# Kernel optimization log

Measured on AMD Instinct MI355X. Metric: run time of the kernel, lower is better.

## Reference

```python
import jax, jax.numpy as jnp
import numpy as np

SIGMA_DATA = 16.0
ALPHA_BOND = 1.0


def safe_norm(x, axis=-1):
    # L2 norm with zero (sub)gradient at 0, matching torch.norm's behavior
    sq = jnp.sum(x * x, axis=axis)
    n = jnp.sqrt(jnp.where(sq > 0, sq, 1.0))
    return jnp.where(sq > 0, n, 0.0)


def weighted_rigid_align(x_l, xGT_l, w_l):
    # Aligns x_l onto xGT_l's frame (Kabsch with weights); output is detached.
    wm = w_l[..., None]                                   # [B,N,1]
    denom = jnp.sum(wm, axis=1, keepdims=True)
    mu = jnp.sum(wm * x_l, axis=1, keepdims=True) / denom
    muGT = jnp.sum(wm * xGT_l, axis=1, keepdims=True) / denom
    xc = x_l - mu
    xGTc = xGT_l - muGT
    # M = (w * xGT_c)^T @ x_c  -> [B,3,3]
    M = jnp.einsum('bni,bnj->bij', wm * xGTc, xc)
    U, S, Vh = jnp.linalg.svd(M)
    R = U @ Vh
    det = jnp.linalg.det(R)
    Fm = jnp.array([[1.0, 0.0, 0.0], [0.0, 1.0, 0.0], [0.0, 0.0, -1.0]], dtype=R.dtype)
    Rfix = jnp.einsum('bij,jk,bkl->bil', U, Fm, Vh)
    R = jnp.where(det[:, None, None] < 0, Rfix, R)
    xalign = xc @ jnp.swapaxes(R, -1, -2) + muGT
    return jax.lax.stop_gradient(xalign)


def diffusion_loss(xpred_l, xGT_l, ht, w_l):
    # Align ground truth onto prediction (note arg order in original forward)
    xGT_aligned = weighted_rigid_align(xGT_l, xpred_l, w_l)
    loss = jnp.sum(safe_norm(xpred_l - xGT_aligned) * w_l) / jnp.sum(w_l)
    if ALPHA_BOND > 0:
        w_pair = w_l[:, :, None] * w_l[:, None, :]                 # [B,N,N]
        d_pred = safe_norm(xpred_l[:, :, None] - xpred_l[:, None]) # [B,N,N]
        d_gt = safe_norm(xGT_l[:, :, None] - xGT_l[:, None])       # [B,N,N]
        L_bond = w_pair * (d_pred - d_gt) ** 2
        loss = loss + ALPHA_BOND * jnp.sum(L_bond) / jnp.sum(w_pair)
    return (ht ** 2 + SIGMA_DATA ** 2) / (ht + SIGMA_DATA) ** 2 * loss


def setup_inputs() -> dict:
    key = jax.random.key(0)
    k1, k2, k3, k4 = jax.random.split(key, 4)
    B, N = 4, 2048
    xpred_l = jax.random.normal(k1, (B, N, 3), dtype=jnp.float32) * 10.0
    xGT_l = jax.random.normal(k2, (B, N, 3), dtype=jnp.float32) * 10.0
    ht = jax.random.uniform(k3, (B,), dtype=jnp.float32, minval=0.1, maxval=4.0)
    w_l = jax.random.uniform(k4, (B, N), dtype=jnp.float32, minval=0.1, maxval=1.0)
    return {"xpred_l": xpred_l, "xGT_l": xGT_l, "ht": ht, "w_l": w_l}


def reference(xpred_l, xGT_l, ht, w_l):
    return diffusion_loss(xpred_l, xGT_l, ht, w_l)
```

## Files before the change

kernel.cpp:

```cpp
#include <hip/hip_runtime.h>
#include <math.h>


#define RT 256
#define CT 64
#define MAXB 8

__global__ __launch_bounds__(RT, 4)
void k_main(const float* __restrict__ pred, const float* __restrict__ gt,
            const float* __restrict__ ht, const float* __restrict__ w,
            float* __restrict__ out, double* __restrict__ ws,
            int N, int B, unsigned total) {
    const int b   = blockIdx.z;
    const int r0  = blockIdx.x * RT;
    const int c0  = blockIdx.y * CT;
    const int tid = threadIdx.x;
    const int lane = tid & 63, wave = tid >> 6;
    const float* p  = pred + (size_t)b * N * 3;
    const float* g  = gt   + (size_t)b * N * 3;
    const float* wb = w    + (size_t)b * N;
    double* stats = ws + (size_t)b * 16;
    double* bondp = ws + 16 * B;
    unsigned* cnt = (unsigned*)(ws + 16 * B + 1);

    __shared__ float4 sp4[CT], sg4[CT];
    __shared__ double shred[4][16];

    const bool bond_active = (c0 + CT > r0 + 1);

    const int n = r0 + tid;
    const bool row_ok = (n < N);
    float px=0.f,py=0.f,pz=0.f,gx=0.f,gy=0.f,gz=0.f,wn=0.f;
    if (row_ok) {
        px = p[3*n]; py = p[3*n+1]; pz = p[3*n+2];
        gx = g[3*n]; gy = g[3*n+1]; gz = g[3*n+2];
        wn = wb[n];
    }

    if (bond_active) {
        for (int i = tid; i < CT; i += RT) {
            int m = c0 + i;
            if (m < N) {
                sp4[i] = make_float4(p[3*m], p[3*m+1], p[3*m+2], wb[m]);
                sg4[i] = make_float4(g[3*m], g[3*m+1], g[3*m+2], 0.0f);
            } else {
                sp4[i] = make_float4(0.f,0.f,0.f,0.f);
                sg4[i] = make_float4(0.f,0.f,0.f,0.f);
            }
        }
        __syncthreads();
    }

    float bond_f = 0.0f;
    if (bond_active && row_ok && (c0 + CT - 1 > n)) {
        int cc = min(CT, N - c0);
        for (int i = 0; i < cc; i++) {
            float4 cp = sp4[i];
            float4 cg = sg4[i];
            float dxp = px-cp.x, dyp = py-cp.y, dzp = pz-cp.z;
            float dp  = sqrtf(dxp*dxp + dyp*dyp + dzp*dzp);
            float dxg = gx-cg.x, dyg = gy-cg.y, dzg = gz-cg.z;
            float dg  = sqrtf(dxg*dxg + dyg*dyg + dzg*dzg);
            float dd  = dp - dg;
            float t   = wn * cp.w * dd * dd;
            bond_f += (c0 + i > n) ? t : 0.0f;
        }
    }
    bond_f *= 2.0f;

    if (blockIdx.y == 0) {
        double wd = (double)wn;
        double pxd=px, pyd=py, pzd=pz, gxd=gx, gyd=gy, gzd=gz;
        double st[16];
        st[0]=wd;
        st[1]=wd*pxd;  st[2]=wd*pyd;  st[3]=wd*pzd;
        st[4]=wd*gxd;  st[5]=wd*gyd;  st[6]=wd*gzd;
        st[7]=wd*pxd*gxd;  st[8]=wd*pxd*gyd;  st[9]=wd*pxd*gzd;
        st[10]=wd*pyd*gxd; st[11]=wd*pyd*gyd; st[12]=wd*pyd*gzd;
        st[13]=wd*pzd*gxd; st[14]=wd*pzd*gyd; st[15]=wd*pzd*gzd;
        #pragma unroll
        for (int off = 32; off > 0; off >>= 1) {
            #pragma unroll
            for (int k = 0; k < 16; k++) st[k] += __shfl_down(st[k], off, 64);
        }
        if (lane == 0) {
            #pragma unroll
            for (int k = 0; k < 16; k++) shred[wave][k] = st[k];
        }
        __syncthreads();
        if (tid < 16) {
            double s = shred[0][tid]+shred[1][tid]+shred[2][tid]+shred[3][tid];
            unsafeAtomicAdd(&stats[tid], s);
        }
    }

    double bd = (double)bond_f;
    #pragma unroll
    for (int off = 32; off > 0; off >>= 1) bd += __shfl_down(bd, off, 64);
    __syncthreads();
    if (lane == 0) shred[wave][0] = bd;
    __syncthreads();
    if (tid == 0) {
        double bt = shred[0][0]+shred[1][0]+shred[2][0]+shred[3][0];
        unsafeAtomicAdd(bondp, bt);
    }

    __shared__ int s_last;
    __syncthreads();
    if (tid == 0) {
        __threadfence();
        unsigned old = atomicAdd(cnt, 1u);
        s_last = (old == total - 1u) ? 1 : 0;
    }
    __syncthreads();
    if (!s_last) return;

    __shared__ double Rm[MAXB][16];
    if (tid < B) {
        double s[16];
        double* sb = ws + (size_t)tid * 16;
        for (int k = 0; k < 16; k++) s[k] = unsafeAtomicAdd(&sb[k], 0.0);
        double W = s[0];
        double mup[3] = { s[1]/W, s[2]/W, s[3]/W };
        double mug[3] = { s[4]/W, s[5]/W, s[6]/W };
        double M[3][3];
        for (int i = 0; i < 3; i++)
            for (int j = 0; j < 3; j++)
                M[i][j] = s[7 + i*3 + j] - W * mup[i] * mug[j];

        double A[3][3];
        for (int i = 0; i < 3; i++)
            for (int j = 0; j < 3; j++) {
                double t = 0.0;
                for (int k = 0; k < 3; k++) t += M[k][i] * M[k][j];
                A[i][j] = t;
            }
        double V[3][3] = {{1,0,0},{0,1,0},{0,0,1}};
        for (int sweep = 0; sweep < 8; sweep++) {
            for (int pq = 0; pq < 3; pq++) {
                int pp_ = (pq == 2) ? 1 : 0;
                int qq_ = (pq == 0) ? 1 : 2;
                double apq = A[pp_][qq_];
                if (fabs(apq) < 1e-300) continue;
                double app = A[pp_][pp_], aqq = A[qq_][qq_];
                double theta = (aqq - app) / (2.0 * apq);
                double t = copysign(1.0, theta) / (fabs(theta) + sqrt(theta*theta + 1.0));
                double c = 1.0 / sqrt(t*t + 1.0), sn = t * c;
                A[pp_][pp_] = app - t * apq;
                A[qq_][qq_] = aqq + t * apq;
                A[pp_][qq_] = A[qq_][pp_] = 0.0;
                int r = 3 - pp_ - qq_;
                double arp = A[r][pp_], arq = A[r][qq_];
                A[r][pp_] = A[pp_][r] = c*arp - sn*arq;
                A[r][qq_] = A[qq_][r] = sn*arp + c*arq;
                for (int rr = 0; rr < 3; rr++) {
                    double vp = V[rr][pp_], vq = V[rr][qq_];
                    V[rr][pp_] = c*vp - sn*vq;
                    V[rr][qq_] = sn*vp + c*vq;
                }
            }
        }
        double d[3] = { A[0][0], A[1][1], A[2][2] };
        int idx[3] = {0, 1, 2};
        for (int i = 0; i < 2; i++)
            for (int j = i + 1; j < 3; j++)
                if (d[idx[j]] > d[idx[i]]) { int tt = idx[i]; idx[i] = idx[j]; idx[j] = tt; }
        double u[3][3], v[3][3];
        for (int i = 0; i < 3; i++) {
            int c_ = idx[i];
            double sv = sqrt(fmax(d[c_], 0.0));
            double inv = (sv > 1e-12) ? 1.0 / sv : 0.0;
            for (int r = 0; r < 3; r++) v[i][r] = V[r][c_];
            for (int r = 0; r < 3; r++) {
                double t = 0.0;
                for (int k = 0; k < 3; k++) t += M[r][k] * v[i][k];
                u[i][r] = t * inv;
            }
        }
        double detM = M[0][0]*(M[1][1]*M[2][2] - M[1][2]*M[2][1])
                    - M[0][1]*(M[1][0]*M[2][2] - M[1][2]*M[2][0])
                    + M[0][2]*(M[1][0]*M[2][1] - M[1][1]*M[2][0]);
        double sg2 = (detM < 0.0) ? -1.0 : 1.0;
        double* o = Rm[tid];
        for (int r = 0; r < 3; r++)
            for (int cc2 = 0; cc2 < 3; cc2++)
                o[r*3 + cc2] = u[0][r]*v[0][cc2] + u[1][r]*v[1][cc2] + sg2 * u[2][r]*v[2][cc2];
        for (int i = 0; i < 3; i++) o[9 + i]  = mup[i];
        for (int i = 0; i < 3; i++) o[12 + i] = mug[i];
        o[15] = W;
    }
    __syncthreads();

    double al = 0.0;
    for (int idx2 = tid; idx2 < B * N; idx2 += RT) {
        int bb = idx2 / N, nn = idx2 - bb * N;
        const float* pp = pred + ((size_t)bb * N + nn) * 3;
        const float* gg = gt   + ((size_t)bb * N + nn) * 3;
        double wv = w[(size_t)bb * N + nn];
        const double* o = Rm[bb];
        double xc0 = (double)gg[0]-o[12], xc1 = (double)gg[1]-o[13], xc2 = (double)gg[2]-o[14];
        double ax = o[0]*xc0 + o[1]*xc1 + o[2]*xc2 + o[9];
        double ay = o[3]*xc0 + o[4]*xc1 + o[5]*xc2 + o[10];
        double az = o[6]*xc0 + o[7]*xc1 + o[8]*xc2 + o[11];
        double ex = (double)pp[0]-ax, ey = (double)pp[1]-ay, ez = (double)pp[2]-az;
        double sq = ex*ex + ey*ey + ez*ez;
        al += (sq > 0.0) ? wv * sqrt(sq) : 0.0;
    }
    #pragma unroll
    for (int off = 32; off > 0; off >>= 1) al += __shfl_down(al, off, 64);
    __syncthreads();
    if (lane == 0) shred[wave][1] = al;
    __syncthreads();
    __shared__ double s_loss;
    if (tid == 0) {
        double at = shred[0][1]+shred[1][1]+shred[2][1]+shred[3][1];
        double tw = 0.0, twp = 0.0;
        for (int i = 0; i < B; i++) { double W = Rm[i][15]; tw += W; twp += W*W; }
        double bond = unsafeAtomicAdd(bondp, 0.0);
        s_loss = at / tw + bond / twp;
    }
    __syncthreads();
    if (tid < B) {
        double h = (double)ht[tid];
        out[tid] = (float)(((h*h + 256.0) / ((h + 16.0)*(h + 16.0))) * s_loss);
    }
}

extern "C" void kernel_launch(void* const* d_in, const int* in_sizes, int n_in,
                              void* d_out, int out_size, void* d_ws, size_t ws_size,
                              hipStream_t stream) {
    const float* pred = (const float*)d_in[0];
    const float* gt   = (const float*)d_in[1];
    const float* ht   = (const float*)d_in[2];
    const float* w    = (const float*)d_in[3];
    int B = in_sizes[2];
    int N = in_sizes[3] / B;
    double* ws = (double*)d_ws;
    float* out = (float*)d_out;

    hipMemsetAsync(d_ws, 0, (size_t)(16 * B + 2) * sizeof(double), stream);

    dim3 grid((N + RT - 1) / RT, (N + CT - 1) / CT, B);
    unsigned total = grid.x * grid.y * grid.z;
    k_main<<<grid, dim3(RT), 0, stream>>>(pred, gt, ht, w, out, ws, N, B, total);
}
```

Measured before the change: 107.7 us.

## Widen column tiles, split bond loop by diagonal, use per-block partial slots

Doubles the column tile width to halve the block count, and splits the bond loop into an unmasked path for tiles fully above the diagonal and a masked path for diagonal tiles. Replaces same-address atomics with per-block partial slots that the last block reduces, drops the threadfence, and computes the final alignment term in float with per-batch rotation hoisted out of the loop. It aims to cut contended atomics, block launch overhead and the serialized double-precision tail. In exchange it zeroes a larger workspace, needs shared staging that limits B*GX, and loses some precision in the float alignment sum.

```diff
diff --git a/kernel.cpp b/kernel.cpp
--- a/kernel.cpp
+++ b/kernel.cpp
@@ -3,32 +3,36 @@
 
 
 #define RT 256
-#define CT 64
+#define CT 128
 #define MAXB 8
+#define MAXSTAT 1024
 
 __global__ __launch_bounds__(RT, 4)
 void k_main(const float* __restrict__ pred, const float* __restrict__ gt,
             const float* __restrict__ ht, const float* __restrict__ w,
             float* __restrict__ out, double* __restrict__ ws,
             int N, int B, unsigned total) {
-    const int b   = blockIdx.z;
-    const int r0  = blockIdx.x * RT;
-    const int c0  = blockIdx.y * CT;
-    const int tid = threadIdx.x;
+    const int b    = blockIdx.z;
+    const int bx   = blockIdx.x;
+    const int r0   = bx * RT;
+    const int c0   = blockIdx.y * CT;
+    const int tid  = threadIdx.x;
     const int lane = tid & 63, wave = tid >> 6;
+    const int GX   = gridDim.x;
+    const unsigned linear = (blockIdx.z * gridDim.y + blockIdx.y) * GX + blockIdx.x;
+
+    double* statsSlot = ws;
+    double* bondSlot  = ws + (size_t)B * GX * 16;
+    unsigned* cnt     = (unsigned*)(bondSlot + total);
+
     const float* p  = pred + (size_t)b * N * 3;
     const float* g  = gt   + (size_t)b * N * 3;
     const float* wb = w    + (size_t)b * N;
-    double* stats = ws + (size_t)b * 16;
-    double* bondp = ws + 16 * B;
-    unsigned* cnt = (unsigned*)(ws + 16 * B + 1);
 
     __shared__ float4 sp4[CT], sg4[CT];
     __shared__ double shred[4][16];
 
-    const bool bond_active = (c0 + CT > r0 + 1);
-
-    const int n = r0 + tid;
+    const int  n      = r0 + tid;
     const bool row_ok = (n < N);
     float px=0.f,py=0.f,pz=0.f,gx=0.f,gy=0.f,gz=0.f,wn=0.f;
     if (row_ok) {
@@ -37,47 +41,53 @@
         wn = wb[n];
     }
 
+    const bool bond_active = (c0 + CT > r0 + 1) && (c0 < N);
+    float bond_f = 0.0f;
     if (bond_active) {
         for (int i = tid; i < CT; i += RT) {
             int m = c0 + i;
+            float4 a = make_float4(0.f,0.f,0.f,0.f), c = a;
             if (m < N) {
-                sp4[i] = make_float4(p[3*m], p[3*m+1], p[3*m+2], wb[m]);
-                sg4[i] = make_float4(g[3*m], g[3*m+1], g[3*m+2], 0.0f);
-            } else {
-                sp4[i] = make_float4(0.f,0.f,0.f,0.f);
-                sg4[i] = make_float4(0.f,0.f,0.f,0.f);
-            }
+                a = make_float4(p[3*m], p[3*m+1], p[3*m+2], wb[m]);
+                c = make_float4(g[3*m], g[3*m+1], g[3*m+2], 0.f);
+            }
+            sp4[i] = a; sg4[i] = c;
         }
         __syncthreads();
-    }
-
-    float bond_f = 0.0f;
-    if (bond_active && row_ok && (c0 + CT - 1 > n)) {
-        int cc = min(CT, N - c0);
-        for (int i = 0; i < cc; i++) {
-            float4 cp = sp4[i];
-            float4 cg = sg4[i];
-            float dxp = px-cp.x, dyp = py-cp.y, dzp = pz-cp.z;
-            float dp  = sqrtf(dxp*dxp + dyp*dyp + dzp*dzp);
-            float dxg = gx-cg.x, dyg = gy-cg.y, dzg = gz-cg.z;
-            float dg  = sqrtf(dxg*dxg + dyg*dyg + dzg*dzg);
-            float dd  = dp - dg;
-            float t   = wn * cp.w * dd * dd;
-            bond_f += (c0 + i > n) ? t : 0.0f;
+        if (row_ok) {
+            const int cc = min(CT, N - c0);
+            if (c0 >= r0 + RT) {
+                for (int i = 0; i < cc; i++) {
+                    float4 cp = sp4[i], cg = sg4[i];
+                    float dxp=px-cp.x, dyp=py-cp.y, dzp=pz-cp.z;
+                    float dxg=gx-cg.x, dyg=gy-cg.y, dzg=gz-cg.z;
+                    float dp = sqrtf(dxp*dxp+dyp*dyp+dzp*dzp);
+                    float dg = sqrtf(dxg*dxg+dyg*dyg+dzg*dzg);
+                    float dd = dp - dg;
+                    bond_f += (wn*cp.w)*(dd*dd);
+                }
+            } else if (n < c0 + cc - 1) {
+                for (int i = 0; i < cc; i++) {
+                    float4 cp = sp4[i], cg = sg4[i];
+                    float dxp=px-cp.x, dyp=py-cp.y, dzp=pz-cp.z;
+                    float dxg=gx-cg.x, dyg=gy-cg.y, dzg=gz-cg.z;
+                    float dp = sqrtf(dxp*dxp+dyp*dyp+dzp*dzp);
+                    float dg = sqrtf(dxg*dxg+dyg*dyg+dzg*dzg);
+                    float dd = dp - dg;
+                    float t  = (wn*cp.w)*(dd*dd);
+                    bond_f += (c0 + i > n) ? t : 0.0f;
+                }
+            }
         }
     }
     bond_f *= 2.0f;
 
     if (blockIdx.y == 0) {
-        double wd = (double)wn;
-        double pxd=px, pyd=py, pzd=pz, gxd=gx, gyd=gy, gzd=gz;
-        double st[16];
-        st[0]=wd;
-        st[1]=wd*pxd;  st[2]=wd*pyd;  st[3]=wd*pzd;
-        st[4]=wd*gxd;  st[5]=wd*gyd;  st[6]=wd*gzd;
-        st[7]=wd*pxd*gxd;  st[8]=wd*pxd*gyd;  st[9]=wd*pxd*gzd;
-        st[10]=wd*pyd*gxd; st[11]=wd*pyd*gyd; st[12]=wd*pyd*gzd;
-        st[13]=wd*pzd*gxd; st[14]=wd*pzd*gyd; st[15]=wd*pzd*gzd;
+        double wd=wn, pxd=px,pyd=py,pzd=pz, gxd=gx,gyd=gy,gzd=gz;
+        double st[16] = {wd, wd*pxd, wd*pyd, wd*pzd, wd*gxd, wd*gyd, wd*gzd,
+                         wd*pxd*gxd, wd*pxd*gyd, wd*pxd*gzd,
+                         wd*pyd*gxd, wd*pyd*gyd, wd*pyd*gzd,
+                         wd*pzd*gxd, wd*pzd*gyd, wd*pzd*gzd};
         #pragma unroll
         for (int off = 32; off > 0; off >>= 1) {
             #pragma unroll
@@ -90,36 +100,52 @@
         __syncthreads();
         if (tid < 16) {
             double s = shred[0][tid]+shred[1][tid]+shred[2][tid]+shred[3][tid];
-            unsafeAtomicAdd(&stats[tid], s);
-        }
+            unsafeAtomicAdd(&statsSlot[((size_t)b*GX + bx)*16 + tid], s);
+        }
+        __syncthreads();
     }
 
     double bd = (double)bond_f;
     #pragma unroll
     for (int off = 32; off > 0; off >>= 1) bd += __shfl_down(bd, off, 64);
-    __syncthreads();
     if (lane == 0) shred[wave][0] = bd;
     __syncthreads();
-    if (tid == 0) {
+    if (tid == 0 && bond_active) {
         double bt = shred[0][0]+shred[1][0]+shred[2][0]+shred[3][0];
-        unsafeAtomicAdd(bondp, bt);
-    }
-
-    __shared__ int s_last;
-    __syncthreads();
-    if (tid == 0) {
-        __threadfence();
-        unsigned old = atomicAdd(cnt, 1u);
-        s_last = (old == total - 1u) ? 1 : 0;
-    }
-    __syncthreads();
-    if (!s_last) return;
-
-    __shared__ double Rm[MAXB][16];
+        unsafeAtomicAdd(&bondSlot[linear], bt);
+    }
+
+    __shared__ unsigned s_old;
+    __syncthreads();
+    if (tid == 0) s_old = atomicAdd(cnt, 1u);
+    __syncthreads();
+    if (s_old != total - 1u) return;
+
+    const int nstat = B * GX * 16;
+    __shared__ double sstat[MAXSTAT];
+    for (int i = tid; i < nstat; i += RT)
+        sstat[i] = unsafeAtomicAdd(&statsSlot[i], 0.0);
+
+    double bsum = 0.0;
+    for (unsigned i = tid; i < total; i += RT)
+        bsum += unsafeAtomicAdd(&bondSlot[i], 0.0);
+    #pragma unroll
+    for (int off = 32; off > 0; off >>= 1) bsum += __shfl_down(bsum, off, 64);
+    if (lane == 0) shred[wave][1] = bsum;
+    __syncthreads();
+
+    __shared__ double s_bond;
+    __shared__ float  Rf[MAXB][15];
+    __shared__ double Wd[MAXB];
+    if (tid == 0) s_bond = shred[0][1]+shred[1][1]+shred[2][1]+shred[3][1];
+
     if (tid < B) {
         double s[16];
-        double* sb = ws + (size_t)tid * 16;
-        for (int k = 0; k < 16; k++) s[k] = unsafeAtomicAdd(&sb[k], 0.0);
+        for (int k = 0; k < 16; k++) {
+            double acc = 0.0;
+            for (int j = 0; j < GX; j++) acc += sstat[((size_t)tid*GX + j)*16 + k];
+            s[k] = acc;
+        }
         double W = s[0];
         double mup[3] = { s[1]/W, s[2]/W, s[3]/W };
         double mug[3] = { s[4]/W, s[5]/W, s[6]/W };
@@ -145,18 +171,18 @@
                 double app = A[pp_][pp_], aqq = A[qq_][qq_];
                 double theta = (aqq - app) / (2.0 * apq);
                 double t = copysign(1.0, theta) / (fabs(theta) + sqrt(theta*theta + 1.0));
-                double c = 1.0 / sqrt(t*t + 1.0), sn = t * c;
+                double cj = 1.0 / sqrt(t*t + 1.0), sn = t * cj;
                 A[pp_][pp_] = app - t * apq;
                 A[qq_][qq_] = aqq + t * apq;
                 A[pp_][qq_] = A[qq_][pp_] = 0.0;
                 int r = 3 - pp_ - qq_;
                 double arp = A[r][pp_], arq = A[r][qq_];
-                A[r][pp_] = A[pp_][r] = c*arp - sn*arq;
-                A[r][qq_] = A[qq_][r] = sn*arp + c*arq;
+                A[r][pp_] = A[pp_][r] = cj*arp - sn*arq;
+                A[r][qq_] = A[qq_][r] = sn*arp + cj*arq;
                 for (int rr = 0; rr < 3; rr++) {
                     double vp = V[rr][pp_], vq = V[rr][qq_];
-                    V[rr][pp_] = c*vp - sn*vq;
-                    V[rr][qq_] = sn*vp + c*vq;
+                    V[rr][pp_] = cj*vp - sn*vq;
+                    V[rr][qq_] = sn*vp + cj*vq;
                 }
             }
         }
@@ -181,43 +207,47 @@
                     - M[0][1]*(M[1][0]*M[2][2] - M[1][2]*M[2][0])
                     + M[0][2]*(M[1][0]*M[2][1] - M[1][1]*M[2][0]);
         double sg2 = (detM < 0.0) ? -1.0 : 1.0;
-        double* o = Rm[tid];
         for (int r = 0; r < 3; r++)
             for (int cc2 = 0; cc2 < 3; cc2++)
-                o[r*3 + cc2] = u[0][r]*v[0][cc2] + u[1][r]*v[1][cc2] + sg2 * u[2][r]*v[2][cc2];
-        for (int i = 0; i < 3; i++) o[9 + i]  = mup[i];
-        for (int i = 0; i < 3; i++) o[12 + i] = mug[i];
-        o[15] = W;
+                Rf[tid][r*3+cc2] = (float)(u[0][r]*v[0][cc2] + u[1][r]*v[1][cc2]
+                                           + sg2 * u[2][r]*v[2][cc2]);
+        for (int i = 0; i < 3; i++) Rf[tid][9 + i]  = (float)mup[i];
+        for (int i = 0; i < 3; i++) Rf[tid][12 + i] = (float)mug[i];
+        Wd[tid] = W;
     }
     __syncthreads();
 
     double al = 0.0;
-    for (int idx2 = tid; idx2 < B * N; idx2 += RT) {
-        int bb = idx2 / N, nn = idx2 - bb * N;
-        const float* pp = pred + ((size_t)bb * N + nn) * 3;
-        const float* gg = gt   + ((size_t)bb * N + nn) * 3;
-        double wv = w[(size_t)bb * N + nn];
-        const double* o = Rm[bb];
-        double xc0 = (double)gg[0]-o[12], xc1 = (double)gg[1]-o[13], xc2 = (double)gg[2]-o[14];
-        double ax = o[0]*xc0 + o[1]*xc1 + o[2]*xc2 + o[9];
-        double ay = o[3]*xc0 + o[4]*xc1 + o[5]*xc2 + o[10];
-        double az = o[6]*xc0 + o[7]*xc1 + o[8]*xc2 + o[11];
-        double ex = (double)pp[0]-ax, ey = (double)pp[1]-ay, ez = (double)pp[2]-az;
-        double sq = ex*ex + ey*ey + ez*ez;
-        al += (sq > 0.0) ? wv * sqrt(sq) : 0.0;
+    for (int bb = 0; bb < B; bb++) {
+        float R0=Rf[bb][0], R1=Rf[bb][1], R2=Rf[bb][2];
+        float R3=Rf[bb][3], R4=Rf[bb][4], R5=Rf[bb][5];
+        float R6=Rf[bb][6], R7=Rf[bb][7], R8=Rf[bb][8];
+        float mp0=Rf[bb][9], mp1=Rf[bb][10], mp2=Rf[bb][11];
+        float mg0=Rf[bb][12], mg1=Rf[bb][13], mg2=Rf[bb][14];
+        const float* pp  = pred + (size_t)bb * N * 3;
+        const float* gg  = gt   + (size_t)bb * N * 3;
+        const float* wwb = w    + (size_t)bb * N;
+        for (int nn = tid; nn < N; nn += RT) {
+            float x0 = gg[3*nn]-mg0, x1 = gg[3*nn+1]-mg1, x2 = gg[3*nn+2]-mg2;
+            float ax = fmaf(R0,x0, fmaf(R1,x1, fmaf(R2,x2, mp0)));
+            float ay = fmaf(R3,x0, fmaf(R4,x1, fmaf(R5,x2, mp1)));
+            float az = fmaf(R6,x0, fmaf(R7,x1, fmaf(R8,x2, mp2)));
+            float ex = pp[3*nn]-ax, ey = pp[3*nn+1]-ay, ez = pp[3*nn+2]-az;
+            float sq = ex*ex + ey*ey + ez*ez;
+            al += (double)(wwb[nn] * sqrtf(sq));
+        }
     }
     #pragma unroll
     for (int off = 32; off > 0; off >>= 1) al += __shfl_down(al, off, 64);
-    __syncthreads();
-    if (lane == 0) shred[wave][1] = al;
-    __syncthreads();
+    if (lane == 0) shred[wave][2] = al;
+    __syncthreads();
+
     __shared__ double s_loss;
     if (tid == 0) {
-        double at = shred[0][1]+shred[1][1]+shred[2][1]+shred[3][1];
+        double at = shred[0][2]+shred[1][2]+shred[2][2]+shred[3][2];
         double tw = 0.0, twp = 0.0;
-        for (int i = 0; i < B; i++) { double W = Rm[i][15]; tw += W; twp += W*W; }
-        double bond = unsafeAtomicAdd(bondp, 0.0);
-        s_loss = at / tw + bond / twp;
+        for (int i = 0; i < B; i++) { double W = Wd[i]; tw += W; twp += W*W; }
+        s_loss = at / tw + s_bond / twp;
     }
     __syncthreads();
     if (tid < B) {
@@ -238,9 +268,11 @@
     double* ws = (double*)d_ws;
     float* out = (float*)d_out;
 
-    hipMemsetAsync(d_ws, 0, (size_t)(16 * B + 2) * sizeof(double), stream);
-
-    dim3 grid((N + RT - 1) / RT, (N + CT - 1) / CT, B);
-    unsigned total = grid.x * grid.y * grid.z;
-    k_main<<<grid, dim3(RT), 0, stream>>>(pred, gt, ht, w, out, ws, N, B, total);
+    int gx = (N + RT - 1) / RT;
+    int gy = (N + CT - 1) / CT;
+    unsigned total = (unsigned)(gx * gy * B);
+    size_t zbytes = ((size_t)B * gx * 16 + total + 2) * sizeof(double);
+    hipMemsetAsync(d_ws, 0, zbytes, stream);
+
+    k_main<<<dim3(gx, gy, B), dim3(RT), 0, stream>>>(pred, gt, ht, w, out, ws, N, B, total);
 }
```

Result: no change. 105.8 us (-1.8%).
